# Performance work log

Measured on AMD Instinct MI355X. Metric: run time of the kernel, lower is better.

Reference implementation:

```python
import jax, jax.numpy as jnp
import numpy as np

N, D, H1, H2, C, K = 8192, 512, 1024, 512, 10, 64
EPS_BN = 1e-5  # torch BatchNorm1d default eps


def _bn(x, g, b):
    # BatchNorm1d in training mode: per-batch stats, biased variance
    mu = x.mean(axis=0)
    var = x.var(axis=0)
    return (x - mu) / jnp.sqrt(var + EPS_BN) * g + b


def _features(x, ibn_g, ibn_b, W1, b1, g1, bb1, W2, b2, g2, bb2):
    x = _bn(x, ibn_g, ibn_b)                    # input_norm
    h = _bn(jnp.tanh(x @ W1.T + b1), g1, bb1)   # layer 1: Linear -> Tanh -> BN
    h = _bn(jnp.tanh(h @ W2.T + b2), g2, bb2)   # layer 2
    return h                                    # [N, H2]


def _nona_self(fx, fn, y_ohe):
    # sim = -cdist(fx, fn); self-neighbor path (x == x_n): -inf diag + top-k mask
    sq_x = jnp.sum(fx * fx, axis=1)
    sq_n = jnp.sum(fn * fn, axis=1)
    d2 = jnp.maximum(sq_x[:, None] + sq_n[None, :] - 2.0 * (fx @ fn.T), 0.0)
    safe = d2 > 1e-9
    dist = jnp.where(safe, jnp.sqrt(jnp.where(safe, d2, 1.0)), 0.0)
    sim = -dist
    eye = jnp.eye(N, dtype=bool)
    sim = jnp.where(eye, -jnp.inf, sim)         # sim -= inf * I
    _, idx = jax.lax.top_k(sim, K)              # [N, K]
    keep = jnp.zeros((N, N), dtype=bool).at[jnp.arange(N)[:, None], idx].set(True)
    sim = jnp.where(keep, sim, -jnp.inf)        # KNNMask: non-topk -> -inf
    probs = jax.nn.softmax(sim, axis=1)
    return jnp.clip(probs @ y_ohe, 0.0, 1.0)


def setup_inputs() -> dict:
    key = jax.random.key(0)
    ks = jax.random.split(key, 6)
    x = jax.random.normal(ks[0], (N, D), dtype=jnp.float32)
    x_n = x + 0.0  # NONA self-neighbor mode requires x_n == x elementwise
    y_n = jax.random.randint(ks[1], (N,), 0, C, dtype=jnp.int32)
    s1 = 1.0 / np.sqrt(D)
    s2 = 1.0 / np.sqrt(H1)
    W1 = jax.random.uniform(ks[2], (H1, D), jnp.float32, -s1, s1)
    b1 = jax.random.uniform(ks[3], (H1,), jnp.float32, -s1, s1)
    W2 = jax.random.uniform(ks[4], (H2, H1), jnp.float32, -s2, s2)
    b2 = jax.random.uniform(ks[5], (H2,), jnp.float32, -s2, s2)
    return {
        "x": x, "x_n": x_n, "y_n": y_n,
        "ibn_g": jnp.ones((D,), jnp.float32), "ibn_b": jnp.zeros((D,), jnp.float32),
        "W1": W1, "b1": b1, "g1": jnp.ones((H1,), jnp.float32), "bb1": jnp.zeros((H1,), jnp.float32),
        "W2": W2, "b2": b2, "g2": jnp.ones((H2,), jnp.float32), "bb2": jnp.zeros((H2,), jnp.float32),
    }


def reference(x, x_n, y_n, ibn_g, ibn_b, W1, b1, g1, bb1, W2, b2, g2, bb2):
    fx = _features(x, ibn_g, ibn_b, W1, b1, g1, bb1, W2, b2, g2, bb2)
    fn = _features(x_n, ibn_g, ibn_b, W1, b1, g1, bb1, W2, b2, g2, bb2)
    y_ohe = jax.nn.one_hot(y_n, C, dtype=jnp.float32)
    return _nona_self(fx, fn, y_ohe)
```

## Files before the change

kernel.cpp:

```cpp
#include <hip/hip_runtime.h>
#include <math.h>

#define NROWS 8192
#define DIM   512
#define HID1  1024
#define HID2  512
#define NCLS  10
#define KTOP  64
#define KPACK 1024
#define KFULL 1536
#define EPSBAND 0.02f

typedef __attribute__((ext_vector_type(8))) short short8;
typedef __attribute__((ext_vector_type(4))) float f32x4;
typedef __attribute__((ext_vector_type(4))) double f64x4;

__device__ __forceinline__ unsigned short f2bf(float x) {
    unsigned u = __float_as_uint(x);
    u += 0x7FFFu + ((u >> 16) & 1u);
    return (unsigned short)(u >> 16);
}
__device__ __forceinline__ float bf2f(unsigned short h) {
    return __uint_as_float(((unsigned)h) << 16);
}

template <typename T>
__global__ __launch_bounds__(256) void col_stats_partial(
    const T* __restrict__ A, int F, int rowsPerBlock,
    double* __restrict__ pSum, double* __restrict__ pSqs)
{
    int c  = blockIdx.x * 256 + threadIdx.x;
    int r0 = blockIdx.y * rowsPerBlock;
    double s = 0.0, s2 = 0.0;
    for (int r = r0; r < r0 + rowsPerBlock; ++r) {
        double v = (double)A[(size_t)r * F + c];
        s  += v;
        s2 += v * v;
    }
    pSum[(size_t)blockIdx.y * F + c] = s;
    pSqs[(size_t)blockIdx.y * F + c] = s2;
}

__global__ __launch_bounds__(256) void col_stats_final(
    const double* __restrict__ pSum, const double* __restrict__ pSqs,
    const float* __restrict__ g, const float* __restrict__ b,
    double* __restrict__ scale, double* __restrict__ shift, int F, int nPart)
{
    int c = blockIdx.x * 256 + threadIdx.x;
    double s = 0.0, s2 = 0.0;
    for (int p = 0; p < nPart; ++p) {
        s  += pSum[(size_t)p * F + c];
        s2 += pSqs[(size_t)p * F + c];
    }
    double mean = s * (1.0 / NROWS);
    double var  = s2 * (1.0 / NROWS) - mean * mean;
    double sc   = (double)g[c] / sqrt(var + 1e-5);
    scale[c] = sc;
    shift[c] = (double)b[c] - mean * sc;
}

__global__ __launch_bounds__(256) void bn_apply_f32(
    const float* __restrict__ x, const double* __restrict__ scl, const double* __restrict__ sft,
    double* __restrict__ out)
{
    const int base = (blockIdx.x * 256 + threadIdx.x) * 4;
    float4 v = *(const float4*)&x[base];
    const int c = base & (DIM - 1);
    out[base + 0] = (double)v.x * scl[c + 0] + sft[c + 0];
    out[base + 1] = (double)v.y * scl[c + 1] + sft[c + 1];
    out[base + 2] = (double)v.z * scl[c + 2] + sft[c + 2];
    out[base + 3] = (double)v.w * scl[c + 3] + sft[c + 3];
}

__global__ __launch_bounds__(256) void bn_apply_f64(
    double* __restrict__ y, const double* __restrict__ scl, const double* __restrict__ sft,
    int mask)
{
    const int base = (blockIdx.x * 256 + threadIdx.x) * 4;
    const int c = base & mask;
    double2 v0 = *(const double2*)&y[base];
    double2 v1 = *(const double2*)&y[base + 2];
    v0.x = v0.x * scl[c + 0] + sft[c + 0];
    v0.y = v0.y * scl[c + 1] + sft[c + 1];
    v1.x = v1.x * scl[c + 2] + sft[c + 2];
    v1.y = v1.y * scl[c + 3] + sft[c + 3];
    *(double2*)&y[base]     = v0;
    *(double2*)&y[base + 2] = v1;
}

__global__ __launch_bounds__(256) void gemm_mfma_tanh(
    const double* __restrict__ A, const float* __restrict__ W, const float* __restrict__ bias,
    double* __restrict__ out, int Kd, int F)
{
    __shared__ double aS[2][16 * 132];
    __shared__ float  bS[2][16 * 68];
    const int t = threadIdx.x;
    const int lane = t & 63;
    const int wv = t >> 6;
    const int nwg = gridDim.x;
    const int q = nwg >> 3;
    const int bid = blockIdx.x;
    const int wgid = (bid & 7) * q + (bid >> 3);
    const int fBlocks = F >> 6;
    const int mb = wgid / fBlocks;
    const int fb = wgid - mb * fBlocks;
    const int fBase = fb * 64;
    const int mBase = mb * 128;
    const int arow = t >> 1;
    const int akq  = (t & 1) * 8;
    const int wrow = t >> 2;
    const int wkq  = (t & 3) * 4;

    f64x4 acc[2][4];
    #pragma unroll
    for (int p = 0; p < 2; ++p)
        #pragma unroll
        for (int n = 0; n < 4; ++n) acc[p][n] = (f64x4){0.0, 0.0, 0.0, 0.0};

    double areg[8];
    float  wreg[4];

    auto stage_load = [&](int ch) {
        const int kb = ch << 4;
        const double* ap = &A[(size_t)(mBase + arow) * Kd + kb + akq];
        #pragma unroll
        for (int j = 0; j < 4; ++j) {
            double2 v = *(const double2*)(ap + 2 * j);
            areg[2 * j] = v.x; areg[2 * j + 1] = v.y;
        }
        float4 w0 = *(const float4*)&W[(size_t)(fBase + wrow) * Kd + kb + wkq];
        wreg[0] = w0.x; wreg[1] = w0.y; wreg[2] = w0.z; wreg[3] = w0.w;
    };
    auto stage_write = [&](int buf) {
        #pragma unroll
        for (int i = 0; i < 8; ++i)
            aS[buf][(akq + i) * 132 + arow] = areg[i];
        #pragma unroll
        for (int i = 0; i < 4; ++i)
            bS[buf][(wkq + i) * 68 + wrow] = wreg[i];
    };
    auto compute = [&](int buf) {
        #pragma unroll
        for (int k4 = 0; k4 < 4; ++k4) {
            const int kk = k4 * 4 + (lane >> 4);
            double a0 = aS[buf][kk * 132 + wv * 16 + (lane & 15)];
            double a1 = aS[buf][kk * 132 + 64 + wv * 16 + (lane & 15)];
            #pragma unroll
            for (int n = 0; n < 4; ++n) {
                double b = (double)bS[buf][kk * 68 + n * 16 + (lane & 15)];
                acc[0][n] = __builtin_amdgcn_mfma_f64_16x16x4f64(a0, b, acc[0][n], 0, 0, 0);
                acc[1][n] = __builtin_amdgcn_mfma_f64_16x16x4f64(a1, b, acc[1][n], 0, 0, 0);
            }
        }
    };

    const int nChunks = Kd >> 4;
    stage_load(0);
    stage_write(0);
    __syncthreads();
    int cur = 0;
    for (int ch = 0; ch < nChunks; ++ch) {
        const bool hn = (ch + 1 < nChunks);
        if (hn) stage_load(ch + 1);
        compute(cur);
        if (hn) stage_write(cur ^ 1);
        __syncthreads();
        cur ^= 1;
    }

    #pragma unroll
    for (int p = 0; p < 2; ++p) {
        #pragma unroll
        for (int n = 0; n < 4; ++n) {
            const int f = fBase + n * 16 + (lane & 15);
            const double bz = (double)bias[f];
            #pragma unroll
            for (int r = 0; r < 4; ++r) {
                const int m = mBase + p * 64 + wv * 16 + (lane >> 4) * 4 + r;
                out[(size_t)m * F + f] = tanh(acc[p][n][r] + bz);
            }
        }
    }
}

__global__ __launch_bounds__(256) void pack_features(
    const double* __restrict__ y2, const double* __restrict__ scl, const double* __restrict__ sft,
    unsigned short* __restrict__ R, float* __restrict__ sqf)
{
    __shared__ double red[4];
    const int r = blockIdx.x;
    const int t = threadIdx.x;
    const int wid = t >> 6, lane = t & 63;
    const int c = t * 2;
    double2 y  = *(const double2*)&y2[(size_t)r * HID2 + c];
    double2 s2 = *(const double2*)&scl[c];
    double2 h2 = *(const double2*)&sft[c];
    double f0 = y.x * s2.x + h2.x;
    double f1 = y.y * s2.y + h2.y;
    unsigned short hi0 = f2bf((float)f0);
    unsigned short hi1 = f2bf((float)f1);
    unsigned short lo0 = f2bf((float)(f0 - (double)bf2f(hi0)));
    unsigned short lo1 = f2bf((float)(f1 - (double)bf2f(hi1)));
    unsigned short* Rr = R + (size_t)r * KPACK;
    Rr[c]           = hi0; Rr[c + 1]           = hi1;
    Rr[HID2 + c]    = lo0; Rr[HID2 + c + 1]    = lo1;
    double s = f0 * f0 + f1 * f1;
    #pragma unroll
    for (int off = 32; off > 0; off >>= 1) s += __shfl_down(s, off);
    if (lane == 0) red[wid] = s;
    __syncthreads();
    if (t == 0) sqf[r] = (float)(red[0] + red[1] + red[2] + red[3]);
}

__global__ __launch_bounds__(256, 1) void sim_mfma(
    const unsigned short* __restrict__ R, const float* __restrict__ sqf,
    float* __restrict__ simbuf, int rowBase)
{
    __shared__ unsigned short aT[2][128 * 64];
    __shared__ unsigned short bT[2][256 * 64];
    const int t = threadIdx.x;
    const int wid = t >> 6, lane = t & 63;
    const int wr = wid >> 1, wc = wid & 1;
    const int bid  = blockIdx.x;
    const int wgid = (bid & 7) * 32 + (bid >> 3);
    const int ib = wgid & 7;
    const int jb = wgid >> 3;
    const int iBase = rowBase + ib * 128;
    const int jBase = jb * 256;
    const int srow = lane >> 3;
    const int skk  = (((lane & 7) ^ srow) * 8);

    f32x4 acc[4][8];
    #pragma unroll
    for (int m = 0; m < 4; ++m)
        #pragma unroll
        for (int n = 0; n < 8; ++n) acc[m][n] = (f32x4){0.f, 0.f, 0.f, 0.f};

    auto STAGE = [&](int buf, int kt) {
        const int k0 = kt * 64;
        const int aSrc = (k0 < 512)  ? k0 : (k0 - 512);
        const int bSrc = (k0 < 1024) ? k0 : (k0 - 1024);
        #pragma unroll
        for (int c = 0; c < 4; ++c) {
            const int g = wid * 4 + c;
            const unsigned short* gp = R + (size_t)(iBase + g * 8 + srow) * KPACK + aSrc + skk;
            __builtin_amdgcn_global_load_lds((const __attribute__((address_space(1))) void*)gp,
                (__attribute__((address_space(3))) void*)&aT[buf][g * 512], 16, 0, 0);
        }
        #pragma unroll
        for (int c = 0; c < 8; ++c) {
            const int g = wid * 8 + c;
            const unsigned short* gp = R + (size_t)(jBase + g * 8 + srow) * KPACK + bSrc + skk;
            __builtin_amdgcn_global_load_lds((const __attribute__((address_space(1))) void*)gp,
                (__attribute__((address_space(3))) void*)&bT[buf][g * 512], 16, 0, 0);
        }
    };
    auto MFMA_TILE = [&](int buf) {
        #pragma unroll
        for (int ks = 0; ks < 2; ++ks) {
            const int ck = ((ks * 4 + (lane >> 4)) ^ (lane & 7)) * 8;
            short8 aF[4], bF[8];
            #pragma unroll
            for (int m = 0; m < 4; ++m) {
                int rA = wr * 64 + m * 16 + (lane & 15);
                aF[m] = *(const short8*)&aT[buf][rA * 64 + ck];
            }
            #pragma unroll
            for (int n = 0; n < 8; ++n) {
                int rB = wc * 128 + n * 16 + (lane & 15);
                bF[n] = *(const short8*)&bT[buf][rB * 64 + ck];
            }
            __builtin_amdgcn_s_setprio(1);
            #pragma unroll
            for (int m = 0; m < 4; ++m)
                #pragma unroll
                for (int n = 0; n < 8; ++n)
                    acc[m][n] = __builtin_amdgcn_mfma_f32_16x16x32_bf16(aF[m], bF[n], acc[m][n], 0, 0, 0);
            __builtin_amdgcn_s_setprio(0);
        }
    };

    const int nKT = KFULL / 64;
    STAGE(0, 0);
    int cur = 0;
    for (int kt = 0; kt < nKT - 1; ++kt) {
        STAGE(cur ^ 1, kt + 1);
        asm volatile("s_waitcnt vmcnt(12)" ::: "memory");
        __builtin_amdgcn_s_barrier();
        asm volatile("" ::: "memory");
        __builtin_amdgcn_sched_barrier(0);
        MFMA_TILE(cur);
        asm volatile("" ::: "memory");
        __builtin_amdgcn_s_barrier();
        cur ^= 1;
    }
    asm volatile("s_waitcnt vmcnt(0)" ::: "memory");
    __builtin_amdgcn_s_barrier();
    asm volatile("" ::: "memory");
    __builtin_amdgcn_sched_barrier(0);
    MFMA_TILE(cur);

    #pragma unroll
    for (int m = 0; m < 4; ++m) {
        #pragma unroll
        for (int n = 0; n < 8; ++n) {
            int j = jBase + wc * 128 + n * 16 + (lane & 15);
            float sqj = sqf[j];
            #pragma unroll
            for (int r = 0; r < 4; ++r) {
                int i = iBase + wr * 64 + m * 16 + (lane >> 4) * 4 + r;
                float d2 = sqf[i] + sqj - 2.0f * acc[m][n][r];
                d2 = fmaxf(d2, 0.f);
                float s = (i == j) ? -INFINITY : -d2;
                simbuf[(size_t)(i - rowBase) * NROWS + j] = s;
            }
        }
    }
}

__device__ __forceinline__ unsigned fKey(float v) {
    unsigned b = __float_as_uint(v);
    return (b & 0x80000000u) ? ~b : (b | 0x80000000u);
}
__device__ __forceinline__ float keyToFloat(unsigned k) {
    unsigned b = (k & 0x80000000u) ? (k ^ 0x80000000u) : ~k;
    return __uint_as_float(b);
}

__global__ __launch_bounds__(256) void topk_refine(
    const float* __restrict__ simbuf,
    const double* __restrict__ y2, const double* __restrict__ scl, const double* __restrict__ sft,
    const int* __restrict__ labels, float* __restrict__ out, int rowBase)
{
    __shared__ unsigned redU[4], redL[4];
    __shared__ int      totArr[36];
    __shared__ float    redF[4];
    __shared__ float    cls[NCLS];
    __shared__ int      bandJ[128];
    __shared__ double   bandD2[128];
    __shared__ unsigned char keepB[128];
    __shared__ int      bandCnt;

    const int t = threadIdx.x;
    const int wid = t >> 6, lane = t & 63;
    const int row = blockIdx.x;
    const int gi = rowBase + row;
    const float* srow = simbuf + (size_t)row * NROWS;

    unsigned key[32];
    #pragma unroll
    for (int ii = 0; ii < 8; ++ii) {
        float4 v = ((const float4*)srow)[t + ii * 256];
        key[ii * 4 + 0] = fKey(v.x);
        key[ii * 4 + 1] = fKey(v.y);
        key[ii * 4 + 2] = fKey(v.z);
        key[ii * 4 + 3] = fKey(v.w);
    }
    const unsigned infKey = fKey(-INFINITY);

    unsigned kmax = 0u, kmin = 0xFFFFFFFFu;
    #pragma unroll
    for (int ii = 0; ii < 32; ++ii) {
        kmax = max(kmax, key[ii]);
        kmin = min(kmin, (key[ii] == infKey) ? 0xFFFFFFFFu : key[ii]);
    }
    #pragma unroll
    for (int off = 32; off > 0; off >>= 1) {
        kmax = max(kmax, (unsigned)__shfl_down(kmax, off));
        kmin = min(kmin, (unsigned)__shfl_down(kmin, off));
    }
    if (lane == 0) { redU[wid] = kmax; redL[wid] = kmin; }
    if (t == 0) bandCnt = 0;
    if (t < NCLS) cls[t] = 0.f;
    if (t < 36) totArr[t] = 0;
    __syncthreads();
    kmax = max(max(redU[0], redU[1]), max(redU[2], redU[3]));
    kmin = min(min(redL[0], redL[1]), min(redL[2], redL[3]));
    float d2min = fmaxf(-keyToFloat(kmax), 0.f);
    float distMin = (d2min > 1e-9f) ? sqrtf(d2min) : 0.f;

    unsigned lo = kmin, hi = kmax;
    int it = 0;
    while (lo < hi) {
        unsigned mid = lo + ((hi - lo + 1u) >> 1);
        int cnt = 0;
        #pragma unroll
        for (int ii = 0; ii < 32; ++ii) cnt += (key[ii] >= mid) ? 1 : 0;
        #pragma unroll
        for (int off = 32; off > 0; off >>= 1) cnt += __shfl_down(cnt, off);
        if (lane == 0) atomicAdd(&totArr[it], cnt);
        __syncthreads();
        int tot = totArr[it];
        if (tot >= KTOP) lo = mid; else hi = mid - 1u;
        ++it;
    }
    const float s64 = keyToFloat(lo);
    const unsigned Ku = fKey(s64 + EPSBAND);
    const unsigned Kl = fKey(s64 - EPSBAND);

    {
        int cnt = 0;
        #pragma unroll
        for (int ii = 0; ii < 32; ++ii) cnt += (key[ii] >= Ku) ? 1 : 0;
        #pragma unroll
        for (int off = 32; off > 0; off >>= 1) cnt += __shfl_down(cnt, off);
        if (lane == 0) atomicAdd(&totArr[34], cnt);
    }
    #pragma unroll
    for (int ii = 0; ii < 8; ++ii) {
        #pragma unroll
        for (int q2 = 0; q2 < 4; ++q2) {
            unsigned k = key[ii * 4 + q2];
            if (k >= Kl && k < Ku) {
                int pos = atomicAdd(&bandCnt, 1);
                if (pos < 128) bandJ[pos] = (t + ii * 256) * 4 + q2;
            }
        }
    }
    __syncthreads();
    const int nSafe = totArr[34];
    const int Rslots = KTOP - nSafe;
    const int nb = min(bandCnt, 128);

    for (int c2 = wid; c2 < nb; c2 += 4) {
        int j = bandJ[c2];
        double s = 0.0;
        for (int d = lane; d < HID2; d += 64) {
            double sc = scl[d], sh = sft[d];
            double fi = y2[(size_t)gi * HID2 + d] * sc + sh;
            double fj = y2[(size_t)j  * HID2 + d] * sc + sh;
            double df = fi - fj;
            s += df * df;
        }
        #pragma unroll
        for (int off = 32; off > 0; off >>= 1) s += __shfl_down(s, off);
        if (lane == 0) bandD2[c2] = s;
    }
    __syncthreads();

    for (int c2 = t; c2 < nb; c2 += 256) {
        double d2c = bandD2[c2];
        int jc = bandJ[c2];
        int rank = 0;
        for (int q2 = 0; q2 < nb; ++q2) {
            double dq = bandD2[q2];
            rank += (dq < d2c || (dq == d2c && bandJ[q2] < jc)) ? 1 : 0;
        }
        keepB[c2] = (rank < Rslots) ? 1 : 0;
    }
    __syncthreads();

    float S = 0.f;
    #pragma unroll
    for (int ii = 0; ii < 8; ++ii) {
        #pragma unroll
        for (int q2 = 0; q2 < 4; ++q2) {
            unsigned k = key[ii * 4 + q2];
            if (k >= Ku) {
                float d2 = -keyToFloat(k);
                float dist = (d2 > 1e-9f) ? sqrtf(d2) : 0.f;
                float w = expf(distMin - dist);
                S += w;
                atomicAdd(&cls[labels[(t + ii * 256) * 4 + q2]], w);
            }
        }
    }
    for (int c2 = t; c2 < nb; c2 += 256) {
        if (keepB[c2]) {
            double dd = bandD2[c2];
            float dist = (dd > 1e-9) ? (float)sqrt(dd) : 0.f;
            float w = expf(distMin - dist);
            S += w;
            atomicAdd(&cls[labels[bandJ[c2]]], w);
        }
    }
    #pragma unroll
    for (int off = 32; off > 0; off >>= 1) S += __shfl_down(S, off);
    if (lane == 0) redF[wid] = S;
    __syncthreads();
    float Stot = redF[0] + redF[1] + redF[2] + redF[3];

    if (t < NCLS) {
        float p = cls[t] / Stot;
        out[(size_t)gi * NCLS + t] = fminf(fmaxf(p, 0.f), 1.f);
    }
}

extern "C" void kernel_launch(void* const* d_in, const int* in_sizes, int n_in,
                              void* d_out, int out_size, void* d_ws, size_t ws_size,
                              hipStream_t stream)
{
    const float* x     = (const float*)d_in[0];
    const int*   y_n   = (const int*)d_in[2];
    const float* ibn_g = (const float*)d_in[3];
    const float* ibn_b = (const float*)d_in[4];
    const float* W1    = (const float*)d_in[5];
    const float* b1    = (const float*)d_in[6];
    const float* g1    = (const float*)d_in[7];
    const float* bb1   = (const float*)d_in[8];
    const float* W2    = (const float*)d_in[9];
    const float* b2    = (const float*)d_in[10];
    const float* g2    = (const float*)d_in[11];
    const float* bb2   = (const float*)d_in[12];
    float* out = (float*)d_out;

    char* ws = (char*)d_ws;
    double*         y1   = (double*)(ws);
    float*          simb = (float*)(ws);
    unsigned short* Rp   = (unsigned short*)(ws + 33554432);
    double*         y2   = (double*)(ws + 67108864);
    double*         xbn  = y2;
    double*         pSum = (double*)(ws + 100663296);
    double*         pSqs = (double*)(ws + 101187584);
    double*         prm  = (double*)(ws + 101711872);
    double* scale0 = prm;           double* shift0 = prm + 1024;
    double* scale1 = prm + 2048;    double* shift1 = prm + 3072;
    double* scale2 = prm + 4096;    double* shift2 = prm + 5120;
    float*          sqf  = (float*)(ws + 101761024);

    dim3 blk(256);
    const int RPB = NROWS / 64;

    col_stats_partial<float><<<dim3(DIM / 256, 64), blk, 0, stream>>>(x, DIM, RPB, pSum, pSqs);
    col_stats_final<<<dim3(DIM / 256), blk, 0, stream>>>(pSum, pSqs, ibn_g, ibn_b, scale0, shift0, DIM, 64);
    bn_apply_f32<<<dim3(NROWS * DIM / 1024), blk, 0, stream>>>(x, scale0, shift0, xbn);
    gemm_mfma_tanh<<<dim3((NROWS / 128) * (HID1 / 64)), blk, 0, stream>>>(xbn, W1, b1, y1, DIM, HID1);
    col_stats_partial<double><<<dim3(HID1 / 256, 64), blk, 0, stream>>>(y1, HID1, RPB, pSum, pSqs);
    col_stats_final<<<dim3(HID1 / 256), blk, 0, stream>>>(pSum, pSqs, g1, bb1, scale1, shift1, HID1, 64);
    bn_apply_f64<<<dim3(NROWS * HID1 / 1024), blk, 0, stream>>>(y1, scale1, shift1, HID1 - 1);
    gemm_mfma_tanh<<<dim3((NROWS / 128) * (HID2 / 64)), blk, 0, stream>>>(y1, W2, b2, y2, HID1, HID2);
    col_stats_partial<double><<<dim3(HID2 / 256, 64), blk, 0, stream>>>(y2, HID2, RPB, pSum, pSqs);
    col_stats_final<<<dim3(HID2 / 256), blk, 0, stream>>>(pSum, pSqs, g2, bb2, scale2, shift2, HID2, 64);
    pack_features<<<dim3(NROWS), blk, 0, stream>>>(y2, scale2, shift2, Rp, sqf);
    for (int ch = 0; ch < 8; ++ch) {
        int rowBase = ch * 1024;
        sim_mfma<<<dim3(256), blk, 0, stream>>>(Rp, sqf, simb, rowBase);
        topk_refine<<<dim3(1024), blk, 0, stream>>>(simb, y2, scale2, shift2, y_n, out, rowBase);
    }
}
```

Baseline: 1.362 ms.

## Use direct global-to-LDS async loads with swizzled layout in FP64 tanh GEMM

The FP64 MFMA GEMM for the MLP layers now stages A and W tiles with global_load_lds straight into XOR-swizzled row-major LDS buffers, replacing the register round trip and transposed padded stores. The K chunk doubles from 16 to 32, and the loop uses an explicit vmcnt wait, barriers and raised wave priority around compute. This targets register staging overhead and LDS bank conflicts, but adds reliance on hand-written waitcnt counts. It also removes empty asm memory clobbers in the distance GEMM, which could let the compiler reorder LDS accesses around the barriers.

```diff
diff --git a/kernel.cpp b/kernel.cpp
--- a/kernel.cpp
+++ b/kernel.cpp
@@ -14,6 +14,9 @@
 typedef __attribute__((ext_vector_type(8))) short short8;
 typedef __attribute__((ext_vector_type(4))) float f32x4;
 typedef __attribute__((ext_vector_type(4))) double f64x4;
+
+#define AS1 __attribute__((address_space(1)))
+#define AS3 __attribute__((address_space(3)))
 
 __device__ __forceinline__ unsigned short f2bf(float x) {
     unsigned u = __float_as_uint(x);
@@ -92,8 +95,8 @@
     const double* __restrict__ A, const float* __restrict__ W, const float* __restrict__ bias,
     double* __restrict__ out, int Kd, int F)
 {
-    __shared__ double aS[2][16 * 132];
-    __shared__ float  bS[2][16 * 68];
+    __shared__ double aD[2][128 * 32];
+    __shared__ float  bD[2][64 * 32];
     const int t = threadIdx.x;
     const int lane = t & 63;
     const int wv = t >> 6;
@@ -106,10 +109,6 @@
     const int fb = wgid - mb * fBlocks;
     const int fBase = fb * 64;
     const int mBase = mb * 128;
-    const int arow = t >> 1;
-    const int akq  = (t & 1) * 8;
-    const int wrow = t >> 2;
-    const int wkq  = (t & 3) * 4;
 
     f64x4 acc[2][4];
     #pragma unroll
@@ -117,56 +116,63 @@
         #pragma unroll
         for (int n = 0; n < 4; ++n) acc[p][n] = (f64x4){0.0, 0.0, 0.0, 0.0};
 
-    double areg[8];
-    float  wreg[4];
-
-    auto stage_load = [&](int ch) {
-        const int kb = ch << 4;
-        const double* ap = &A[(size_t)(mBase + arow) * Kd + kb + akq];
-        #pragma unroll
-        for (int j = 0; j < 4; ++j) {
-            double2 v = *(const double2*)(ap + 2 * j);
-            areg[2 * j] = v.x; areg[2 * j + 1] = v.y;
-        }
-        float4 w0 = *(const float4*)&W[(size_t)(fBase + wrow) * Kd + kb + wkq];
-        wreg[0] = w0.x; wreg[1] = w0.y; wreg[2] = w0.z; wreg[3] = w0.w;
+    auto STAGE = [&](int buf, int ch) {
+        const int kb = ch << 5;
+        #pragma unroll
+        for (int i = 0; i < 8; ++i) {
+            const int cid = (wv * 8 + i) * 64 + lane;
+            const int row = cid >> 4, cl = cid & 15;
+            const int cs = cl ^ (row & 7);
+            const double* gp = &A[(size_t)(mBase + row) * Kd + kb + cs * 2];
+            __builtin_amdgcn_global_load_lds((const AS1 void*)gp,
+                (AS3 void*)&aD[buf][(wv * 8 + i) * 128], 16, 0, 0);
+        }
+        #pragma unroll
+        for (int j = 0; j < 2; ++j) {
+            const int cid = (wv * 2 + j) * 64 + lane;
+            const int col = cid >> 3, cl = cid & 7;
+            const int cs = cl ^ (col & 7);
+            const float* gp = &W[(size_t)(fBase + col) * Kd + kb + cs * 4];
+            __builtin_amdgcn_global_load_lds((const AS1 void*)gp,
+                (AS3 void*)&bD[buf][(wv * 2 + j) * 256], 16, 0, 0);
+        }
     };
-    auto stage_write = [&](int buf) {
-        #pragma unroll
-        for (int i = 0; i < 8; ++i)
-            aS[buf][(akq + i) * 132 + arow] = areg[i];
-        #pragma unroll
-        for (int i = 0; i < 4; ++i)
-            bS[buf][(wkq + i) * 68 + wrow] = wreg[i];
-    };
-    auto compute = [&](int buf) {
-        #pragma unroll
-        for (int k4 = 0; k4 < 4; ++k4) {
+    auto COMPUTE = [&](int buf) {
+        #pragma unroll
+        for (int k4 = 0; k4 < 8; ++k4) {
             const int kk = k4 * 4 + (lane >> 4);
-            double a0 = aS[buf][kk * 132 + wv * 16 + (lane & 15)];
-            double a1 = aS[buf][kk * 132 + 64 + wv * 16 + (lane & 15)];
+            const int r0 = wv * 16 + (lane & 15);
+            const int sw = ((kk >> 1) ^ (r0 & 7)) * 2 + (kk & 1);
+            double a0 = aD[buf][r0 * 32 + sw];
+            double a1 = aD[buf][(r0 + 64) * 32 + sw];
             #pragma unroll
             for (int n = 0; n < 4; ++n) {
-                double b = (double)bS[buf][kk * 68 + n * 16 + (lane & 15)];
+                const int cl = n * 16 + (lane & 15);
+                double b = (double)bD[buf][cl * 32 + ((kk >> 2) ^ (cl & 7)) * 4 + (kk & 3)];
                 acc[0][n] = __builtin_amdgcn_mfma_f64_16x16x4f64(a0, b, acc[0][n], 0, 0, 0);
                 acc[1][n] = __builtin_amdgcn_mfma_f64_16x16x4f64(a1, b, acc[1][n], 0, 0, 0);
             }
         }
     };
 
-    const int nChunks = Kd >> 4;
-    stage_load(0);
-    stage_write(0);
-    __syncthreads();
+    const int nChunks = Kd >> 5;
+    STAGE(0, 0);
     int cur = 0;
-    for (int ch = 0; ch < nChunks; ++ch) {
-        const bool hn = (ch + 1 < nChunks);
-        if (hn) stage_load(ch + 1);
-        compute(cur);
-        if (hn) stage_write(cur ^ 1);
-        __syncthreads();
+    for (int ch = 0; ch < nChunks - 1; ++ch) {
+        STAGE(cur ^ 1, ch + 1);
+        asm volatile("s_waitcnt vmcnt(10)" ::: "memory");
+        __builtin_amdgcn_s_barrier();
+        __builtin_amdgcn_sched_barrier(0);
+        __builtin_amdgcn_s_setprio(1);
+        COMPUTE(cur);
+        __builtin_amdgcn_s_setprio(0);
+        __builtin_amdgcn_s_barrier();
         cur ^= 1;
     }
+    asm volatile("s_waitcnt vmcnt(0)" ::: "memory");
+    __builtin_amdgcn_s_barrier();
+    __builtin_amdgcn_sched_barrier(0);
+    COMPUTE(cur);
 
     #pragma unroll
     for (int p = 0; p < 2; ++p) {
@@ -244,15 +250,15 @@
         for (int c = 0; c < 4; ++c) {
             const int g = wid * 4 + c;
             const unsigned short* gp = R + (size_t)(iBase + g * 8 + srow) * KPACK + aSrc + skk;
-            __builtin_amdgcn_global_load_lds((const __attribute__((address_space(1))) void*)gp,
-                (__attribute__((address_space(3))) void*)&aT[buf][g * 512], 16, 0, 0);
+            __builtin_amdgcn_global_load_lds((const AS1 void*)gp,
+                (AS3 void*)&aT[buf][g * 512], 16, 0, 0);
         }
         #pragma unroll
         for (int c = 0; c < 8; ++c) {
             const int g = wid * 8 + c;
             const unsigned short* gp = R + (size_t)(jBase + g * 8 + srow) * KPACK + bSrc + skk;
-            __builtin_amdgcn_global_load_lds((const __attribute__((address_space(1))) void*)gp,
-                (__attribute__((address_space(3))) void*)&bT[buf][g * 512], 16, 0, 0);
+            __builtin_amdgcn_global_load_lds((const AS1 void*)gp,
+                (AS3 void*)&bT[buf][g * 512], 16, 0, 0);
         }
     };
     auto MFMA_TILE = [&](int buf) {
@@ -287,16 +293,13 @@
         STAGE(cur ^ 1, kt + 1);
         asm volatile("s_waitcnt vmcnt(12)" ::: "memory");
         __builtin_amdgcn_s_barrier();
-        asm volatile("" ::: "memory");
         __builtin_amdgcn_sched_barrier(0);
         MFMA_TILE(cur);
-        asm volatile("" ::: "memory");
         __builtin_amdgcn_s_barrier();
         cur ^= 1;
     }
     asm volatile("s_waitcnt vmcnt(0)" ::: "memory");
     __builtin_amdgcn_s_barrier();
-    asm volatile("" ::: "memory");
     __builtin_amdgcn_sched_barrier(0);
     MFMA_TILE(cur);
 
```

New measurement: 1.276 ms. -6.4%, faster.
